# Kernel tuning notes

Hardware: AMD Instinct MI355X
Metric: run time of the kernel (lower is better)

Reference implementation:

```python
import jax, jax.numpy as jnp
import numpy as np

B, T = 256, 2048
D = 64           # rnn_embd_dims (== input_dims)
LB = 2           # len(band_names)
DB = D // LB     # band_embedding_dims = 32
L = 2            # rnn_layers
G = 3 * DB       # GRU gate width


def setup_inputs() -> dict:
    key = jax.random.key(0)
    ks = jax.random.split(key, 10)
    s = 0.1
    return {
        "band_ids": jax.random.randint(ks[0], (B, T), 0, LB),
        "dtime": jax.random.uniform(ks[1], (B, T, 1), dtype=jnp.float32),
        "z_last": jax.random.normal(ks[2], (B, D), dtype=jnp.float32),
        # per-band params stacked on a leading band axis
        "proj_W": jax.random.normal(ks[3], (LB, D + 1, DB)) * s,
        "proj_b": jnp.zeros((LB, DB)),
        "Wih": jax.random.normal(ks[4], (LB, L, G, DB)) * s,
        "Whh": jax.random.normal(ks[5], (LB, L, G, DB)) * s,
        "bih": jnp.zeros((LB, L, G)),
        "bhh": jnp.zeros((LB, L, G)),
        "mW1": jax.random.normal(ks[6], (LB, DB, DB)) * s,
        "mb1": jnp.zeros((LB, DB)),
        "mW2": jax.random.normal(ks[7], (LB, DB, 1)) * s,
        "mb2": jnp.zeros((LB, 1)),
    }


def _gru_layer(x, mask, Wih, Whh, bih, bhh):
    # x: [B,T,DB], mask: [B,T] bool (True = valid step; invalid steps keep h)
    gx = jnp.einsum('btd,gd->btg', x, Wih) + bih  # precompute input gates [B,T,3*DB]

    def step(h, inp):
        gx_t, m_t = inp                 # [B,G], [B]
        gh = h @ Whh.T + bhh            # [B,G]
        r = jax.nn.sigmoid(gx_t[:, :DB] + gh[:, :DB])
        z = jax.nn.sigmoid(gx_t[:, DB:2 * DB] + gh[:, DB:2 * DB])
        n = jnp.tanh(gx_t[:, 2 * DB:] + r * gh[:, 2 * DB:])
        hn = (1.0 - z) * n + z * h
        h = jnp.where(m_t[:, None], hn, h)
        return h, h

    h0 = jnp.zeros((x.shape[0], DB), x.dtype)
    _, ys = jax.lax.scan(step, h0, (gx.transpose(1, 0, 2), mask.T))
    return ys.transpose(1, 0, 2)  # [B,T,DB]


def _forward(band_ids, dtime, z_last, proj_W, proj_b, Wih, Whh, bih, bhh, mW1, mb1, mW2, mb2):
    Bn, Tn = band_ids.shape
    outs = []
    for kb in range(LB):
        mask = band_ids == kb  # [B,T]
        # serial_to_parallel: stable-compact valid steps to the front of each row
        order = jnp.argsort(jnp.logical_not(mask), axis=1, stable=True)
        p_mask = jnp.take_along_axis(mask, order, axis=1)
        p_dtime = jnp.take_along_axis(dtime, order[:, :, None], axis=1)
        # dz = z_last tiled over t; gather along t is identity for a t-constant tensor
        p_dz = jnp.broadcast_to(z_last[:, None, :], (Bn, Tn, z_last.shape[-1]))
        x = jnp.concatenate([p_dz, p_dtime], axis=-1) @ proj_W[kb] + proj_b[kb]
        for l in range(L):
            x = _gru_layer(x, p_mask, Wih[kb, l], Whh[kb, l], bih[kb, l], bhh[kb, l])
        # dz_projection MLP: hidden relu layer + linear head -> [B,T,1]
        y = jax.nn.relu(x @ mW1[kb] + mb1[kb]) @ mW2[kb] + mb2[kb]
        outs.append(y)
    return tuple(outs)


def reference(band_ids, dtime, z_last, proj_W, proj_b, Wih, Whh, bih, bhh, mW1, mb1, mW2, mb2):
    return _forward(band_ids, dtime, z_last, proj_W, proj_b, Wih, Whh, bih, bhh, mW1, mb1, mW2, mb2)
```

## Files before the change

kernel.cpp:

```cpp
#include <hip/hip_runtime.h>


typedef float v2f __attribute__((ext_vector_type(2)));

constexpr int Bn  = 256;
constexpr int Tn  = 2048;
constexpr int Dn  = 64;
constexpr int DBn = 32;
constexpr int Ln  = 2;
constexpr int Gn  = 96;
constexpr int Kc  = 32;

#if __has_builtin(__builtin_amdgcn_exp2f)
__device__ __forceinline__ float exp2_fast(float x) { return __builtin_amdgcn_exp2f(x); }
#else
__device__ __forceinline__ float exp2_fast(float x) { return exp2f(x); }
#endif
#if __has_builtin(__builtin_amdgcn_rcpf)
__device__ __forceinline__ float rcp_fast(float x) { return __builtin_amdgcn_rcpf(x); }
#else
__device__ __forceinline__ float rcp_fast(float x) { return 1.0f / x; }
#endif

__device__ __forceinline__ float sigmoid_f(float x) {
  return rcp_fast(1.0f + exp2_fast(-1.4426950408889634f * x));
}
__device__ __forceinline__ float tanh_f(float x) {
  return 1.0f - 2.0f * rcp_fast(1.0f + exp2_fast(2.8853900817779268f * x));
}

template <int CTRL>
__device__ __forceinline__ float dpp_add(float x) {
  int y = __builtin_amdgcn_update_dpp(0, __builtin_bit_cast(int, x), CTRL, 0xf, 0xf, true);
  return x + __builtin_bit_cast(float, y);
}
__device__ __forceinline__ float dppx8_add(float x) { return dpp_add<0x128>(x); }
__device__ __forceinline__ float dpp_row_sum16(float x) {
  x = dpp_add<0x128>(x);
  x = dpp_add<0x124>(x);
  x = dpp_add<0x122>(x);
  x = dpp_add<0x121>(x);
  return x;
}

__device__ __forceinline__ float dot8(const v2f* __restrict__ w, const v2f* __restrict__ h) {
  v2f a = {0.0f, 0.0f};
  #pragma unroll
  for (int q = 0; q < 8; ++q) a = __builtin_elementwise_fma(w[q], h[q], a);
  return a.x + a.y;
}
__device__ __forceinline__ float dot8b(const v2f* __restrict__ w, const v2f* __restrict__ h) {
  v2f a = {0.0f, 0.0f}, b = {0.0f, 0.0f};
  #pragma unroll
  for (int q = 0; q < 4; ++q) {
    a = __builtin_elementwise_fma(w[q], h[q], a);
    b = __builtin_elementwise_fma(w[q + 4], h[q + 4], b);
  }
  a = a + b;
  return a.x + a.y;
}

__device__ __forceinline__ void ld16(const float* p, v2f* d) {
  #pragma unroll
  for (int q = 0; q < 4; ++q) {
    float4 a = ((const float4*)p)[q];
    d[2*q] = (v2f){a.x, a.y}; d[2*q+1] = (v2f){a.z, a.w};
  }
}

__global__ __launch_bounds__(256, 1)
void rnn_decoder(const int* __restrict__ band_ids, const float* __restrict__ dtime,
                 const float* __restrict__ z_last, const float* __restrict__ projW,
                 const float* __restrict__ projB, const float* __restrict__ Wih,
                 const float* __restrict__ Whh, const float* __restrict__ bih,
                 const float* __restrict__ bhh, const float* __restrict__ mW1,
                 const float* __restrict__ mb1, const float* __restrict__ mW2,
                 const float* __restrict__ mb2, float* __restrict__ out) {
  const int b    = blockIdx.x >> 1;
  const int kb   = blockIdx.x & 1;
  const int tid  = threadIdx.x;
  const int w    = tid >> 6;
  const int L    = tid & 63;
  const int e    = (L & 7) | ((L >> 4) << 3);
  const int koff = ((L >> 3) & 1) * 16;

  __shared__ __align__(16) float yd[Tn];
  __shared__ __align__(16) float gxr_[2][Kc][DBn][4];
  __shared__ __align__(16) float h1r_[2][Kc][DBn];
  __shared__ __align__(16) float h2r_[2][Kc][DBn];
  __shared__ __align__(16) float vr_[2][Kc][4];
  __shared__ __align__(16) float xb[DBn], xs[DBn];
  __shared__ int nsh;

  const float mb2v = mb2[kb];

  if (w == 0) {
    {
      const int*   brow = band_ids + b * Tn;
      const float* drow = dtime    + b * Tn;
      int cnt = 0;
      int4 bcache[8];
      #pragma unroll
      for (int it = 0; it < 8; ++it) {
        int4 v = ((const int4*)(brow + L * 32))[it];
        bcache[it] = v;
        cnt += (v.x == kb) + (v.y == kb) + (v.z == kb) + (v.w == kb);
      }
      int incl = cnt;
      #pragma unroll
      for (int dlt = 1; dlt < 64; dlt <<= 1) {
        int v = __shfl_up(incl, dlt, 64);
        if (L >= dlt) incl += v;
      }
      int off = incl - cnt;
      const int n0 = __shfl(incl, 63, 64);
      #pragma unroll
      for (int it = 0; it < 8; ++it) {
        int4   v  = bcache[it];
        float4 dd = ((const float4*)(drow + L * 32))[it];
        if (v.x == kb) yd[off++] = dd.x;
        if (v.y == kb) yd[off++] = dd.y;
        if (v.z == kb) yd[off++] = dd.z;
        if (v.w == kb) yd[off++] = dd.w;
      }
      if (L == 0) nsh = n0;
    }
    {
      const float* pw = projW + (kb * (Dn + 1)) * DBn + e;
      const float* zl = z_last + b * Dn;
      float acc = 0.0f;
      #pragma unroll 8
      for (int k = 0; k < Dn; ++k) acc = fmaf(zl[k], pw[k * DBn], acc);
      xb[e] = acc + projB[kb * DBn + e];
      xs[e] = pw[Dn * DBn];
    }
    __builtin_amdgcn_wave_barrier();
    const float* wih1  = Wih + ((kb * Ln + 0) * Gn) * DBn;
    const float* bih1p = bih + (kb * Ln + 0) * Gn;
    const float* bhh1p = bhh + (kb * Ln + 0) * Gn;
    float gb_r = 0, gb_z = 0, gb_n = 0, gs_r = 0, gs_z = 0, gs_n = 0;
    #pragma unroll 4
    for (int j = 0; j < DBn; ++j) {
      float xbv = xb[j], xsv = xs[j];
      float wr = wih1[(     e) * DBn + j];
      float wz = wih1[(32 + e) * DBn + j];
      float wn = wih1[(64 + e) * DBn + j];
      gb_r = fmaf(wr, xbv, gb_r);  gs_r = fmaf(wr, xsv, gs_r);
      gb_z = fmaf(wz, xbv, gb_z);  gs_z = fmaf(wz, xsv, gs_z);
      gb_n = fmaf(wn, xbv, gb_n);  gs_n = fmaf(wn, xsv, gs_n);
    }
    gb_r += bih1p[e]      + bhh1p[e];
    gb_z += bih1p[32 + e] + bhh1p[32 + e];
    gb_n += bih1p[64 + e];
    const float bhh1n = bhh1p[64 + e];
    v2f w1r[8], w1z[8], w1n[8];
    const float* whh1 = Whh + ((kb * Ln + 0) * Gn) * DBn;
    ld16(whh1 + (     e) * DBn + koff, w1r);
    ld16(whh1 + (32 + e) * DBn + koff, w1z);
    ld16(whh1 + (64 + e) * DBn + koff, w1n);
    __syncthreads();

#if __has_builtin(__builtin_amdgcn_s_setprio)
    __builtin_amdgcn_s_setprio(1);
#endif
    const int n = nsh;
    const int C = (n + Kc - 1) >> 5;
    v2f h1a[8];
    #pragma unroll
    for (int q = 0; q < 8; ++q) h1a[q] = (v2f){0.0f, 0.0f};
    float h1self = 0.0f;
    for (int c = 0; c < C + 4; ++c) {
      if (c < C) {
        float* ring = &h1r_[c & 1][0][0];
        const int t0 = c * Kc;
        for (int k = 0; k < Kc; ++k) {
          float d  = yd[t0 + k];
          float ar = dot8b(w1r, h1a);
          float az = dot8b(w1z, h1a);
          float an = dot8b(w1n, h1a);
          ar = dppx8_add(ar);
          az = dppx8_add(az);
          an = dppx8_add(an);
          float r1 = sigmoid_f(fmaf(d, gs_r, gb_r) + ar);
          float z1 = sigmoid_f(fmaf(d, gs_z, gb_z) + az);
          float n1 = tanh_f(fmaf(d, gs_n, gb_n) + r1 * (an + bhh1n));
          h1self = fmaf(z1, h1self - n1, n1);
          ring[k * DBn + e] = h1self;
          __builtin_amdgcn_wave_barrier();
          ld16(&ring[k * DBn + koff], h1a);
        }
      }
      __syncthreads();
    }
  } else if (w == 1) {
    const float* wih2 = Wih + ((kb * Ln + 1) * Gn) * DBn;
    v2f wa[8], wbv[8], wcv[8];
    ld16(wih2 + (     e) * DBn + koff, wa);
    ld16(wih2 + (32 + e) * DBn + koff, wbv);
    ld16(wih2 + (64 + e) * DBn + koff, wcv);
    __syncthreads();

    const int n = nsh;
    const int C = (n + Kc - 1) >> 5;
    for (int c = 0; c < C + 4; ++c) {
      if (c >= 1 && c <= C) {
        const int cp = c - 1;
        const float* hsrc = &h1r_[cp & 1][0][0];
        for (int k = 0; k < Kc; ++k) {
          v2f hb[8];
          ld16(&hsrc[k * DBn + koff], hb);
          float g0 = dot8(wa,  hb);
          float g1 = dot8(wbv, hb);
          float g2 = dot8(wcv, hb);
          g0 = dppx8_add(g0);
          g1 = dppx8_add(g1);
          g2 = dppx8_add(g2);
          float4 gv; gv.x = g0; gv.y = g1; gv.z = g2; gv.w = 0.0f;
          *(float4*)&gxr_[cp & 1][k][e][0] = gv;
        }
      }
      if (c >= 4) {
        const int cd = c - 4;
        if (cd < C && L < 32) {
          float4 p = *(const float4*)&vr_[cd & 1][L][0];
          yd[cd * Kc + L] = ((p.x + p.y) + (p.z + p.w)) + mb2v;
        }
      }
      __syncthreads();
    }
  } else if (w == 2) {
    const float* whh2  = Whh + ((kb * Ln + 1) * Gn) * DBn;
    const float* bih2p = bih + (kb * Ln + 1) * Gn;
    const float* bhh2p = bhh + (kb * Ln + 1) * Gn;
    v2f r2w[8], z2w[8], n2w[8];
    ld16(whh2 + (     e) * DBn + koff, r2w);
    ld16(whh2 + (32 + e) * DBn + koff, z2w);
    ld16(whh2 + (64 + e) * DBn + koff, n2w);
    const float c2r   = bih2p[e]      + bhh2p[e];
    const float c2z   = bih2p[32 + e] + bhh2p[32 + e];
    const float bih2n = bih2p[64 + e];
    const float bhh2n = bhh2p[64 + e];
    __syncthreads();

#if __has_builtin(__builtin_amdgcn_s_setprio)
    __builtin_amdgcn_s_setprio(1);
#endif
    const int n = nsh;
    const int C = (n + Kc - 1) >> 5;
    v2f h2a[8];
    #pragma unroll
    for (int q = 0; q < 8; ++q) h2a[q] = (v2f){0.0f, 0.0f};
    float h2self = 0.0f;
    for (int c = 0; c < C + 4; ++c) {
      if (c >= 2 && c <= C + 1) {
        const int cc = c - 2;
        float* ring = &h2r_[cc & 1][0][0];
        for (int k = 0; k < Kc; ++k) {
          float4 g = *(const float4*)&gxr_[cc & 1][k][e][0];
          float cr = dot8b(r2w, h2a);
          float cz = dot8b(z2w, h2a);
          float cn = dot8b(n2w, h2a);
          cr = dppx8_add(cr);
          cz = dppx8_add(cz);
          cn = dppx8_add(cn);
          float r2v = sigmoid_f(g.x + cr + c2r);
          float z2v = sigmoid_f(g.y + cz + c2z);
          float n2v = tanh_f(g.z + bih2n + r2v * (cn + bhh2n));
          h2self = fmaf(z2v, h2self - n2v, n2v);
          ring[k * DBn + e] = h2self;
          __builtin_amdgcn_wave_barrier();
          ld16(&ring[k * DBn + koff], h2a);
        }
      }
      __syncthreads();
    }
  } else {
    v2f m1c[8];
    #pragma unroll
    for (int q = 0; q < 8; ++q)
      m1c[q] = (v2f){ mW1[(kb * DBn + koff + 2*q)     * DBn + e],
                      mW1[(kb * DBn + koff + 2*q + 1) * DBn + e] };
    const float mb1e = mb1[kb * DBn + e];
    const float mW2h = 0.5f * mW2[kb * DBn + e];
    {
      float p = fmaxf(mb1e, 0.0f) * mW2h;
      p = dpp_row_sum16(p);
      if ((L & 15) == 15) vr_[0][L >> 4][(L >> 4) & 3] = p;
    }
    {
      float p = fmaxf(mb1e, 0.0f) * mW2h;
      p = dpp_row_sum16(p);
      if ((L & 15) == 15) vr_[0][0][L >> 4] = p;
    }
    __syncthreads();

    const int n = nsh;
    const int C = (n + Kc - 1) >> 5;
    for (int c = 0; c < C + 4; ++c) {
      if (c >= 3 && c <= C + 2) {
        const int cm = c - 3;
        const float* hsrc = &h2r_[cm & 1][0][0];
        for (int k = 0; k < Kc; ++k) {
          v2f hb[8];
          ld16(&hsrc[k * DBn + koff], hb);
          float mh = dot8(m1c, hb);
          mh = dppx8_add(mh);
          float v = fmaxf(mh + mb1e, 0.0f) * mW2h;
          v = dpp_row_sum16(v);
          if ((L & 15) == 15) vr_[cm & 1][k][L >> 4] = v;
        }
      }
      __syncthreads();
    }
  }

  const int n = nsh;
  float ylast;
  if (n > 0) {
    ylast = yd[n - 1];
  } else {
    float4 p = *(const float4*)&vr_[0][0][0];
    ylast = ((p.x + p.y) + (p.z + p.w)) + mb2v;
  }
  for (int t = n + tid; t < Tn; t += 256) yd[t] = ylast;
  __syncthreads();

  float* orow = out + (kb * Bn + b) * Tn;
  for (int q = tid; q < Tn / 4; q += 256)
    ((float4*)orow)[q] = ((const float4*)yd)[q];
}

extern "C" void kernel_launch(void* const* d_in, const int* in_sizes, int n_in,
                              void* d_out, int out_size, void* d_ws, size_t ws_size,
                              hipStream_t stream) {
  const int*   band_ids = (const int*)  d_in[0];
  const float* dtime    = (const float*)d_in[1];
  const float* z_last   = (const float*)d_in[2];
  const float* projW    = (const float*)d_in[3];
  const float* projB    = (const float*)d_in[4];
  const float* Wih      = (const float*)d_in[5];
  const float* Whh      = (const float*)d_in[6];
  const float* bihp     = (const float*)d_in[7];
  const float* bhhp     = (const float*)d_in[8];
  const float* mW1      = (const float*)d_in[9];
  const float* mb1      = (const float*)d_in[10];
  const float* mW2      = (const float*)d_in[11];
  const float* mb2      = (const float*)d_in[12];
  float* out = (float*)d_out;
  rnn_decoder<<<dim3(Bn * 2), dim3(256), 0, stream>>>(
      band_ids, dtime, z_last, projW, projB, Wih, Whh, bihp, bhhp,
      mW1, mb1, mW2, mb2, out);
}
```

Measured before the change: 325.5 us.

## Merge four-wave pipeline into two waves fusing input-gate and MLP work

Shrinks each block from four waves to two. The layer-1 recurrence wave also computes the layer-2 input-gate projection from its own hidden state, one step behind. The layer-2 recurrence wave also computes the MLP head output in the same way. The shared-memory hidden-state ring buffers become single-step buffers and the pipeline depth drops from four chunks to two, which cuts barrier stages and LDS traffic. The trade-off is more ALU work on the serial critical-path waves, and setprio is removed.

```diff
diff --git a/kernel.cpp b/kernel.cpp
--- a/kernel.cpp
+++ b/kernel.cpp
@@ -68,7 +68,7 @@
   }
 }
 
-__global__ __launch_bounds__(256, 1)
+__global__ __launch_bounds__(128, 1)
 void rnn_decoder(const int* __restrict__ band_ids, const float* __restrict__ dtime,
                  const float* __restrict__ z_last, const float* __restrict__ projW,
                  const float* __restrict__ projB, const float* __restrict__ Wih,
@@ -86,10 +86,11 @@
 
   __shared__ __align__(16) float yd[Tn];
   __shared__ __align__(16) float gxr_[2][Kc][DBn][4];
-  __shared__ __align__(16) float h1r_[2][Kc][DBn];
-  __shared__ __align__(16) float h2r_[2][Kc][DBn];
   __shared__ __align__(16) float vr_[2][Kc][4];
+  __shared__ __align__(16) float h1b[DBn];
+  __shared__ __align__(16) float h2b[DBn];
   __shared__ __align__(16) float xb[DBn], xs[DBn];
+  __shared__ __align__(16) float y0f[4];
   __shared__ int nsh;
 
   const float mb2v = mb2[kb];
@@ -158,21 +159,23 @@
     ld16(whh1 + (     e) * DBn + koff, w1r);
     ld16(whh1 + (32 + e) * DBn + koff, w1z);
     ld16(whh1 + (64 + e) * DBn + koff, w1n);
+    v2f ua[8], ub[8], uc[8];
+    const float* wih2 = Wih + ((kb * Ln + 1) * Gn) * DBn;
+    ld16(wih2 + (     e) * DBn + koff, ua);
+    ld16(wih2 + (32 + e) * DBn + koff, ub);
+    ld16(wih2 + (64 + e) * DBn + koff, uc);
     __syncthreads();
 
-#if __has_builtin(__builtin_amdgcn_s_setprio)
-    __builtin_amdgcn_s_setprio(1);
-#endif
     const int n = nsh;
     const int C = (n + Kc - 1) >> 5;
     v2f h1a[8];
     #pragma unroll
     for (int q = 0; q < 8; ++q) h1a[q] = (v2f){0.0f, 0.0f};
     float h1self = 0.0f;
-    for (int c = 0; c < C + 4; ++c) {
+    for (int c = 0; c < C + 2; ++c) {
       if (c < C) {
-        float* ring = &h1r_[c & 1][0][0];
         const int t0 = c * Kc;
+        float* gxo = &gxr_[c & 1][0][0][0];
         for (int k = 0; k < Kc; ++k) {
           float d  = yd[t0 + k];
           float ar = dot8b(w1r, h1a);
@@ -184,43 +187,35 @@
           float r1 = sigmoid_f(fmaf(d, gs_r, gb_r) + ar);
           float z1 = sigmoid_f(fmaf(d, gs_z, gb_z) + az);
           float n1 = tanh_f(fmaf(d, gs_n, gb_n) + r1 * (an + bhh1n));
-          h1self = fmaf(z1, h1self - n1, n1);
-          ring[k * DBn + e] = h1self;
+          float h1new = fmaf(z1, h1self - n1, n1);
+          h1b[e] = h1new;
           __builtin_amdgcn_wave_barrier();
-          ld16(&ring[k * DBn + koff], h1a);
-        }
-      }
-      __syncthreads();
-    }
-  } else if (w == 1) {
-    const float* wih2 = Wih + ((kb * Ln + 1) * Gn) * DBn;
-    v2f wa[8], wbv[8], wcv[8];
-    ld16(wih2 + (     e) * DBn + koff, wa);
-    ld16(wih2 + (32 + e) * DBn + koff, wbv);
-    ld16(wih2 + (64 + e) * DBn + koff, wcv);
-    __syncthreads();
-
-    const int n = nsh;
-    const int C = (n + Kc - 1) >> 5;
-    for (int c = 0; c < C + 4; ++c) {
-      if (c >= 1 && c <= C) {
-        const int cp = c - 1;
-        const float* hsrc = &h1r_[cp & 1][0][0];
-        for (int k = 0; k < Kc; ++k) {
-          v2f hb[8];
-          ld16(&hsrc[k * DBn + koff], hb);
-          float g0 = dot8(wa,  hb);
-          float g1 = dot8(wbv, hb);
-          float g2 = dot8(wcv, hb);
+          if (k >= 1) {
+            float g0 = dot8(ua, h1a);
+            float g1 = dot8(ub, h1a);
+            float g2 = dot8(uc, h1a);
+            g0 = dppx8_add(g0);
+            g1 = dppx8_add(g1);
+            g2 = dppx8_add(g2);
+            float4 gv; gv.x = g0; gv.y = g1; gv.z = g2; gv.w = 0.0f;
+            *(float4*)&gxo[(k - 1) * DBn * 4 + e * 4] = gv;
+          }
+          h1self = h1new;
+          ld16(&h1b[koff], h1a);
+        }
+        {
+          float g0 = dot8(ua, h1a);
+          float g1 = dot8(ub, h1a);
+          float g2 = dot8(uc, h1a);
           g0 = dppx8_add(g0);
           g1 = dppx8_add(g1);
           g2 = dppx8_add(g2);
           float4 gv; gv.x = g0; gv.y = g1; gv.z = g2; gv.w = 0.0f;
-          *(float4*)&gxr_[cp & 1][k][e][0] = gv;
-        }
-      }
-      if (c >= 4) {
-        const int cd = c - 4;
+          *(float4*)&gxo[(Kc - 1) * DBn * 4 + e * 4] = gv;
+        }
+      }
+      if (c >= 2) {
+        const int cd = c - 2;
         if (cd < C && L < 32) {
           float4 p = *(const float4*)&vr_[cd & 1][L][0];
           yd[cd * Kc + L] = ((p.x + p.y) + (p.z + p.w)) + mb2v;
@@ -228,35 +223,43 @@
       }
       __syncthreads();
     }
-  } else if (w == 2) {
+  } else {
     const float* whh2  = Whh + ((kb * Ln + 1) * Gn) * DBn;
     const float* bih2p = bih + (kb * Ln + 1) * Gn;
     const float* bhh2p = bhh + (kb * Ln + 1) * Gn;
-    v2f r2w[8], z2w[8], n2w[8];
+    v2f r2w[8], z2w[8], n2w[8], m1c[8];
     ld16(whh2 + (     e) * DBn + koff, r2w);
     ld16(whh2 + (32 + e) * DBn + koff, z2w);
     ld16(whh2 + (64 + e) * DBn + koff, n2w);
+    #pragma unroll
+    for (int q = 0; q < 8; ++q)
+      m1c[q] = (v2f){ mW1[(kb * DBn + koff + 2*q)     * DBn + e],
+                      mW1[(kb * DBn + koff + 2*q + 1) * DBn + e] };
     const float c2r   = bih2p[e]      + bhh2p[e];
     const float c2z   = bih2p[32 + e] + bhh2p[32 + e];
     const float bih2n = bih2p[64 + e];
     const float bhh2n = bhh2p[64 + e];
+    const float mb1e  = mb1[kb * DBn + e];
+    const float mW2h  = 0.5f * mW2[kb * DBn + e];
+    {
+      float p = fmaxf(mb1e, 0.0f) * mW2h;
+      p = dpp_row_sum16(p);
+      if ((L & 15) == 15) y0f[L >> 4] = p;
+    }
     __syncthreads();
 
-#if __has_builtin(__builtin_amdgcn_s_setprio)
-    __builtin_amdgcn_s_setprio(1);
-#endif
     const int n = nsh;
     const int C = (n + Kc - 1) >> 5;
     v2f h2a[8];
     #pragma unroll
     for (int q = 0; q < 8; ++q) h2a[q] = (v2f){0.0f, 0.0f};
     float h2self = 0.0f;
-    for (int c = 0; c < C + 4; ++c) {
-      if (c >= 2 && c <= C + 1) {
-        const int cc = c - 2;
-        float* ring = &h2r_[cc & 1][0][0];
+    for (int c = 0; c < C + 2; ++c) {
+      if (c >= 1 && c <= C) {
+        const int cc = c - 1;
+        const float* gx = &gxr_[cc & 1][0][0][0];
         for (int k = 0; k < Kc; ++k) {
-          float4 g = *(const float4*)&gxr_[cc & 1][k][e][0];
+          float4 g = *(const float4*)&gx[k * DBn * 4 + e * 4];
           float cr = dot8b(r2w, h2a);
           float cz = dot8b(z2w, h2a);
           float cn = dot8b(n2w, h2a);
@@ -266,48 +269,25 @@
           float r2v = sigmoid_f(g.x + cr + c2r);
           float z2v = sigmoid_f(g.y + cz + c2z);
           float n2v = tanh_f(g.z + bih2n + r2v * (cn + bhh2n));
-          h2self = fmaf(z2v, h2self - n2v, n2v);
-          ring[k * DBn + e] = h2self;
+          float h2new = fmaf(z2v, h2self - n2v, n2v);
+          h2b[e] = h2new;
           __builtin_amdgcn_wave_barrier();
-          ld16(&ring[k * DBn + koff], h2a);
-        }
-      }
-      __syncthreads();
-    }
-  } else {
-    v2f m1c[8];
-    #pragma unroll
-    for (int q = 0; q < 8; ++q)
-      m1c[q] = (v2f){ mW1[(kb * DBn + koff + 2*q)     * DBn + e],
-                      mW1[(kb * DBn + koff + 2*q + 1) * DBn + e] };
-    const float mb1e = mb1[kb * DBn + e];
-    const float mW2h = 0.5f * mW2[kb * DBn + e];
-    {
-      float p = fmaxf(mb1e, 0.0f) * mW2h;
-      p = dpp_row_sum16(p);
-      if ((L & 15) == 15) vr_[0][L >> 4][(L >> 4) & 3] = p;
-    }
-    {
-      float p = fmaxf(mb1e, 0.0f) * mW2h;
-      p = dpp_row_sum16(p);
-      if ((L & 15) == 15) vr_[0][0][L >> 4] = p;
-    }
-    __syncthreads();
-
-    const int n = nsh;
-    const int C = (n + Kc - 1) >> 5;
-    for (int c = 0; c < C + 4; ++c) {
-      if (c >= 3 && c <= C + 2) {
-        const int cm = c - 3;
-        const float* hsrc = &h2r_[cm & 1][0][0];
-        for (int k = 0; k < Kc; ++k) {
-          v2f hb[8];
-          ld16(&hsrc[k * DBn + koff], hb);
-          float mh = dot8(m1c, hb);
+          if (k >= 1) {
+            float mh = dot8(m1c, h2a);
+            mh = dppx8_add(mh);
+            float v = fmaxf(mh + mb1e, 0.0f) * mW2h;
+            v = dpp_row_sum16(v);
+            if ((L & 15) == 15) vr_[cc & 1][k - 1][L >> 4] = v;
+          }
+          h2self = h2new;
+          ld16(&h2b[koff], h2a);
+        }
+        {
+          float mh = dot8(m1c, h2a);
           mh = dppx8_add(mh);
           float v = fmaxf(mh + mb1e, 0.0f) * mW2h;
           v = dpp_row_sum16(v);
-          if ((L & 15) == 15) vr_[cm & 1][k][L >> 4] = v;
+          if ((L & 15) == 15) vr_[cc & 1][Kc - 1][L >> 4] = v;
         }
       }
       __syncthreads();
@@ -319,14 +299,14 @@
   if (n > 0) {
     ylast = yd[n - 1];
   } else {
-    float4 p = *(const float4*)&vr_[0][0][0];
+    float4 p = *(const float4*)&y0f[0];
     ylast = ((p.x + p.y) + (p.z + p.w)) + mb2v;
   }
-  for (int t = n + tid; t < Tn; t += 256) yd[t] = ylast;
+  for (int t = n + tid; t < Tn; t += 128) yd[t] = ylast;
   __syncthreads();
 
   float* orow = out + (kb * Bn + b) * Tn;
-  for (int q = tid; q < Tn / 4; q += 256)
+  for (int q = tid; q < Tn / 4; q += 128)
     ((float4*)orow)[q] = ((const float4*)yd)[q];
 }
 
@@ -347,7 +327,7 @@
   const float* mW2      = (const float*)d_in[11];
   const float* mb2      = (const float*)d_in[12];
   float* out = (float*)d_out;
-  rnn_decoder<<<dim3(Bn * 2), dim3(256), 0, stream>>>(
+  rnn_decoder<<<dim3(Bn * 2), dim3(128), 0, stream>>>(
       band_ids, dtime, z_last, projW, projB, Wih, Whh, bihp, bhhp,
       mW1, mb1, mW2, mb2, out);
 }
```

After: 478.3 us. 46.9% more time.

## Fuse MLP head into layer-2 GRU wave and shorten pipeline to three waves

Applied to the files above, without the earlier changes.

The wave that ran the dz-projection MLP is removed. Its MLP is now computed inside the layer-2 GRU wave, one step behind, using a ping-pong of register copies of h2 in place of the h2 shared-memory ring. The block shrinks to 192 threads and the chunk pipeline loses one stage, which reduces pipeline fill/drain and barrier work. The layer-1 loop also reads dtime four steps at a time. The exchange is that the serial layer-2 recurrence now carries extra MLP arithmetic on its critical path.

```diff
diff --git a/kernel.cpp b/kernel.cpp
--- a/kernel.cpp
+++ b/kernel.cpp
@@ -68,7 +68,7 @@
   }
 }
 
-__global__ __launch_bounds__(256, 1)
+__global__ __launch_bounds__(192, 1)
 void rnn_decoder(const int* __restrict__ band_ids, const float* __restrict__ dtime,
                  const float* __restrict__ z_last, const float* __restrict__ projW,
                  const float* __restrict__ projB, const float* __restrict__ Wih,
@@ -87,9 +87,10 @@
   __shared__ __align__(16) float yd[Tn];
   __shared__ __align__(16) float gxr_[2][Kc][DBn][4];
   __shared__ __align__(16) float h1r_[2][Kc][DBn];
-  __shared__ __align__(16) float h2r_[2][Kc][DBn];
   __shared__ __align__(16) float vr_[2][Kc][4];
+  __shared__ __align__(16) float h2b[DBn];
   __shared__ __align__(16) float xb[DBn], xs[DBn];
+  __shared__ __align__(16) float y0f[4];
   __shared__ int nsh;
 
   const float mb2v = mb2[kb];
@@ -169,25 +170,29 @@
     #pragma unroll
     for (int q = 0; q < 8; ++q) h1a[q] = (v2f){0.0f, 0.0f};
     float h1self = 0.0f;
-    for (int c = 0; c < C + 4; ++c) {
+    for (int c = 0; c < C + 3; ++c) {
       if (c < C) {
         float* ring = &h1r_[c & 1][0][0];
         const int t0 = c * Kc;
-        for (int k = 0; k < Kc; ++k) {
-          float d  = yd[t0 + k];
-          float ar = dot8b(w1r, h1a);
-          float az = dot8b(w1z, h1a);
-          float an = dot8b(w1n, h1a);
-          ar = dppx8_add(ar);
-          az = dppx8_add(az);
-          an = dppx8_add(an);
-          float r1 = sigmoid_f(fmaf(d, gs_r, gb_r) + ar);
-          float z1 = sigmoid_f(fmaf(d, gs_z, gb_z) + az);
-          float n1 = tanh_f(fmaf(d, gs_n, gb_n) + r1 * (an + bhh1n));
-          h1self = fmaf(z1, h1self - n1, n1);
-          ring[k * DBn + e] = h1self;
-          __builtin_amdgcn_wave_barrier();
-          ld16(&ring[k * DBn + koff], h1a);
+        for (int k = 0; k < Kc; k += 4) {
+          float4 d4 = *(const float4*)&yd[t0 + k];
+          #pragma unroll
+          for (int u = 0; u < 4; ++u) {
+            float d  = (u == 0) ? d4.x : (u == 1) ? d4.y : (u == 2) ? d4.z : d4.w;
+            float ar = dot8b(w1r, h1a);
+            float az = dot8b(w1z, h1a);
+            float an = dot8b(w1n, h1a);
+            ar = dppx8_add(ar);
+            az = dppx8_add(az);
+            an = dppx8_add(an);
+            float r1 = sigmoid_f(fmaf(d, gs_r, gb_r) + ar);
+            float z1 = sigmoid_f(fmaf(d, gs_z, gb_z) + az);
+            float n1 = tanh_f(fmaf(d, gs_n, gb_n) + r1 * (an + bhh1n));
+            h1self = fmaf(z1, h1self - n1, n1);
+            ring[(k + u) * DBn + e] = h1self;
+            __builtin_amdgcn_wave_barrier();
+            ld16(&ring[(k + u) * DBn + koff], h1a);
+          }
         }
       }
       __syncthreads();
@@ -202,7 +207,7 @@
 
     const int n = nsh;
     const int C = (n + Kc - 1) >> 5;
-    for (int c = 0; c < C + 4; ++c) {
+    for (int c = 0; c < C + 3; ++c) {
       if (c >= 1 && c <= C) {
         const int cp = c - 1;
         const float* hsrc = &h1r_[cp & 1][0][0];
@@ -219,8 +224,8 @@
           *(float4*)&gxr_[cp & 1][k][e][0] = gv;
         }
       }
-      if (c >= 4) {
-        const int cd = c - 4;
+      if (c >= 3) {
+        const int cd = c - 3;
         if (cd < C && L < 32) {
           float4 p = *(const float4*)&vr_[cd & 1][L][0];
           yd[cd * Kc + L] = ((p.x + p.y) + (p.z + p.w)) + mb2v;
@@ -228,18 +233,29 @@
       }
       __syncthreads();
     }
-  } else if (w == 2) {
+  } else {
     const float* whh2  = Whh + ((kb * Ln + 1) * Gn) * DBn;
     const float* bih2p = bih + (kb * Ln + 1) * Gn;
     const float* bhh2p = bhh + (kb * Ln + 1) * Gn;
-    v2f r2w[8], z2w[8], n2w[8];
+    v2f r2w[8], z2w[8], n2w[8], m1c[8];
     ld16(whh2 + (     e) * DBn + koff, r2w);
     ld16(whh2 + (32 + e) * DBn + koff, z2w);
     ld16(whh2 + (64 + e) * DBn + koff, n2w);
+    #pragma unroll
+    for (int q = 0; q < 8; ++q)
+      m1c[q] = (v2f){ mW1[(kb * DBn + koff + 2*q)     * DBn + e],
+                      mW1[(kb * DBn + koff + 2*q + 1) * DBn + e] };
     const float c2r   = bih2p[e]      + bhh2p[e];
     const float c2z   = bih2p[32 + e] + bhh2p[32 + e];
     const float bih2n = bih2p[64 + e];
     const float bhh2n = bhh2p[64 + e];
+    const float mb1e  = mb1[kb * DBn + e];
+    const float mW2h  = 0.5f * mW2[kb * DBn + e];
+    {
+      float p = fmaxf(mb1e, 0.0f) * mW2h;
+      p = dpp_row_sum16(p);
+      if ((L & 15) == 15) y0f[L >> 4] = p;
+    }
     __syncthreads();
 
 #if __has_builtin(__builtin_amdgcn_s_setprio)
@@ -247,71 +263,55 @@
 #endif
     const int n = nsh;
     const int C = (n + Kc - 1) >> 5;
-    v2f h2a[8];
+    v2f h2A[8], h2B[8];
     #pragma unroll
-    for (int q = 0; q < 8; ++q) h2a[q] = (v2f){0.0f, 0.0f};
+    for (int q = 0; q < 8; ++q) { h2A[q] = (v2f){0.0f, 0.0f}; h2B[q] = (v2f){0.0f, 0.0f}; }
     float h2self = 0.0f;
-    for (int c = 0; c < C + 4; ++c) {
+
+#define L2_STEP(K, CUR, NXT)                                                   \
+    {                                                                          \
+      float4 g = *(const float4*)&gxr_[cc & 1][(K)][e][0];                     \
+      float cr = dot8b(r2w, CUR);                                              \
+      float cz = dot8b(z2w, CUR);                                              \
+      float cn = dot8b(n2w, CUR);                                              \
+      cr = dppx8_add(cr);                                                      \
+      cz = dppx8_add(cz);                                                      \
+      cn = dppx8_add(cn);                                                      \
+      float r2v = sigmoid_f(g.x + cr + c2r);                                   \
+      float z2v = sigmoid_f(g.y + cz + c2z);                                   \
+      float n2v = tanh_f(g.z + bih2n + r2v * (cn + bhh2n));                    \
+      float h2new = fmaf(z2v, h2self - n2v, n2v);                              \
+      h2b[e] = h2new;                                                          \
+      __builtin_amdgcn_wave_barrier();                                         \
+      ld16(&h2b[koff], NXT);                                                   \
+      if ((K) >= 1) {                                                          \
+        float mh = dot8(m1c, CUR);                                             \
+        mh = dppx8_add(mh);                                                    \
+        float v = fmaxf(mh + mb1e, 0.0f) * mW2h;                               \
+        v = dpp_row_sum16(v);                                                  \
+        if ((L & 15) == 15) vr_[cc & 1][(K) - 1][L >> 4] = v;                  \
+      }                                                                        \
+      h2self = h2new;                                                          \
+    }
+
+    for (int c = 0; c < C + 3; ++c) {
       if (c >= 2 && c <= C + 1) {
         const int cc = c - 2;
-        float* ring = &h2r_[cc & 1][0][0];
-        for (int k = 0; k < Kc; ++k) {
-          float4 g = *(const float4*)&gxr_[cc & 1][k][e][0];
-          float cr = dot8b(r2w, h2a);
-          float cz = dot8b(z2w, h2a);
-          float cn = dot8b(n2w, h2a);
-          cr = dppx8_add(cr);
-          cz = dppx8_add(cz);
-          cn = dppx8_add(cn);
-          float r2v = sigmoid_f(g.x + cr + c2r);
-          float z2v = sigmoid_f(g.y + cz + c2z);
-          float n2v = tanh_f(g.z + bih2n + r2v * (cn + bhh2n));
-          h2self = fmaf(z2v, h2self - n2v, n2v);
-          ring[k * DBn + e] = h2self;
-          __builtin_amdgcn_wave_barrier();
-          ld16(&ring[k * DBn + koff], h2a);
-        }
-      }
-      __syncthreads();
-    }
-  } else {
-    v2f m1c[8];
-    #pragma unroll
-    for (int q = 0; q < 8; ++q)
-      m1c[q] = (v2f){ mW1[(kb * DBn + koff + 2*q)     * DBn + e],
-                      mW1[(kb * DBn + koff + 2*q + 1) * DBn + e] };
-    const float mb1e = mb1[kb * DBn + e];
-    const float mW2h = 0.5f * mW2[kb * DBn + e];
-    {
-      float p = fmaxf(mb1e, 0.0f) * mW2h;
-      p = dpp_row_sum16(p);
-      if ((L & 15) == 15) vr_[0][L >> 4][(L >> 4) & 3] = p;
-    }
-    {
-      float p = fmaxf(mb1e, 0.0f) * mW2h;
-      p = dpp_row_sum16(p);
-      if ((L & 15) == 15) vr_[0][0][L >> 4] = p;
-    }
-    __syncthreads();
-
-    const int n = nsh;
-    const int C = (n + Kc - 1) >> 5;
-    for (int c = 0; c < C + 4; ++c) {
-      if (c >= 3 && c <= C + 2) {
-        const int cm = c - 3;
-        const float* hsrc = &h2r_[cm & 1][0][0];
-        for (int k = 0; k < Kc; ++k) {
-          v2f hb[8];
-          ld16(&hsrc[k * DBn + koff], hb);
-          float mh = dot8(m1c, hb);
+        for (int k = 0; k < Kc; k += 2) {
+          L2_STEP(k,     h2A, h2B)
+          L2_STEP(k + 1, h2B, h2A)
+        }
+        {
+          float mh = dot8(m1c, h2A);
           mh = dppx8_add(mh);
           float v = fmaxf(mh + mb1e, 0.0f) * mW2h;
           v = dpp_row_sum16(v);
-          if ((L & 15) == 15) vr_[cm & 1][k][L >> 4] = v;
+          if ((L & 15) == 15) vr_[cc & 1][Kc - 1][L >> 4] = v;
         }
       }
       __syncthreads();
     }
+#undef L2_STEP
   }
 
   const int n = nsh;
@@ -319,14 +319,14 @@
   if (n > 0) {
     ylast = yd[n - 1];
   } else {
-    float4 p = *(const float4*)&vr_[0][0][0];
+    float4 p = *(const float4*)&y0f[0];
     ylast = ((p.x + p.y) + (p.z + p.w)) + mb2v;
   }
-  for (int t = n + tid; t < Tn; t += 256) yd[t] = ylast;
+  for (int t = n + tid; t < Tn; t += 192) yd[t] = ylast;
   __syncthreads();
 
   float* orow = out + (kb * Bn + b) * Tn;
-  for (int q = tid; q < Tn / 4; q += 256)
+  for (int q = tid; q < Tn / 4; q += 192)
     ((float4*)orow)[q] = ((const float4*)yd)[q];
 }
 
@@ -347,7 +347,7 @@
   const float* mW2      = (const float*)d_in[11];
   const float* mb2      = (const float*)d_in[12];
   float* out = (float*)d_out;
-  rnn_decoder<<<dim3(Bn * 2), dim3(256), 0, stream>>>(
+  rnn_decoder<<<dim3(Bn * 2), dim3(192), 0, stream>>>(
       band_ids, dtime, z_last, projW, projB, Wih, Whh, bihp, bhhp,
       mW1, mb1, mW2, mb2, out);
 }
```

Measured after the change: 425.4 us. +30.7%, slower.

## Remap lanes so each lane owns two outputs with 4-way K split

Applied to the files above, without the earlier changes.

Changes the per-wave lane mapping from 2-way K split with one output element per lane to a 4-way K split with two output elements per lane (e and e+16). Each lane now does half-length dot products per gate and reduces across 4 lanes with two DPP adds. The recurrent h reload per step shrinks to 8 floats, and the layer-1 loop reads dtime as float4 and unrolls by 4. The aim is to shorten the serial per-step dependency chain in the GRU recurrences, at the cost of twice as many gate activations per lane and more registers.

```diff
diff --git a/kernel.cpp b/kernel.cpp
--- a/kernel.cpp
+++ b/kernel.cpp
@@ -34,38 +34,27 @@
   int y = __builtin_amdgcn_update_dpp(0, __builtin_bit_cast(int, x), CTRL, 0xf, 0xf, true);
   return x + __builtin_bit_cast(float, y);
 }
-__device__ __forceinline__ float dppx8_add(float x) { return dpp_add<0x128>(x); }
-__device__ __forceinline__ float dpp_row_sum16(float x) {
+__device__ __forceinline__ float comb48(float x) {
+  x = dpp_add<0x124>(x);
   x = dpp_add<0x128>(x);
-  x = dpp_add<0x124>(x);
-  x = dpp_add<0x122>(x);
-  x = dpp_add<0x121>(x);
   return x;
 }
 
-__device__ __forceinline__ float dot8(const v2f* __restrict__ w, const v2f* __restrict__ h) {
-  v2f a = {0.0f, 0.0f};
-  #pragma unroll
-  for (int q = 0; q < 8; ++q) a = __builtin_elementwise_fma(w[q], h[q], a);
-  return a.x + a.y;
-}
-__device__ __forceinline__ float dot8b(const v2f* __restrict__ w, const v2f* __restrict__ h) {
+__device__ __forceinline__ float dot4(const v2f* __restrict__ w, const v2f* __restrict__ h) {
   v2f a = {0.0f, 0.0f}, b = {0.0f, 0.0f};
-  #pragma unroll
-  for (int q = 0; q < 4; ++q) {
-    a = __builtin_elementwise_fma(w[q], h[q], a);
-    b = __builtin_elementwise_fma(w[q + 4], h[q + 4], b);
-  }
+  a = __builtin_elementwise_fma(w[0], h[0], a);
+  b = __builtin_elementwise_fma(w[1], h[1], b);
+  a = __builtin_elementwise_fma(w[2], h[2], a);
+  b = __builtin_elementwise_fma(w[3], h[3], b);
   a = a + b;
   return a.x + a.y;
 }
 
-__device__ __forceinline__ void ld16(const float* p, v2f* d) {
-  #pragma unroll
-  for (int q = 0; q < 4; ++q) {
-    float4 a = ((const float4*)p)[q];
-    d[2*q] = (v2f){a.x, a.y}; d[2*q+1] = (v2f){a.z, a.w};
-  }
+__device__ __forceinline__ void ld8(const float* p, v2f* d) {
+  float4 a = ((const float4*)p)[0];
+  float4 bq = ((const float4*)p)[1];
+  d[0] = (v2f){a.x, a.y};  d[1] = (v2f){a.z, a.w};
+  d[2] = (v2f){bq.x, bq.y}; d[3] = (v2f){bq.z, bq.w};
 }
 
 __global__ __launch_bounds__(256, 1)
@@ -81,8 +70,10 @@
   const int tid  = threadIdx.x;
   const int w    = tid >> 6;
   const int L    = tid & 63;
-  const int e    = (L & 7) | ((L >> 4) << 3);
-  const int koff = ((L >> 3) & 1) * 16;
+  const int row  = L >> 4;
+  const int kq   = (L >> 2) & 3;
+  const int e    = (L & 3) | (row << 2);
+  const int ko   = kq * 8;
 
   __shared__ __align__(16) float yd[Tn];
   __shared__ __align__(16) float gxr_[2][Kc][DBn][4];
@@ -90,6 +81,7 @@
   __shared__ __align__(16) float h2r_[2][Kc][DBn];
   __shared__ __align__(16) float vr_[2][Kc][4];
   __shared__ __align__(16) float xb[DBn], xs[DBn];
+  __shared__ __align__(16) float y0f[4];
   __shared__ int nsh;
 
   const float mb2v = mb2[kb];
@@ -126,38 +118,56 @@
       if (L == 0) nsh = n0;
     }
     {
-      const float* pw = projW + (kb * (Dn + 1)) * DBn + e;
       const float* zl = z_last + b * Dn;
-      float acc = 0.0f;
-      #pragma unroll 8
-      for (int k = 0; k < Dn; ++k) acc = fmaf(zl[k], pw[k * DBn], acc);
-      xb[e] = acc + projB[kb * DBn + e];
-      xs[e] = pw[Dn * DBn];
+      #pragma unroll
+      for (int s = 0; s < 2; ++s) {
+        const int ee = e + 16 * s;
+        const float* pw = projW + (kb * (Dn + 1)) * DBn + ee;
+        float acc = 0.0f;
+        #pragma unroll 8
+        for (int k = 0; k < Dn; ++k) acc = fmaf(zl[k], pw[k * DBn], acc);
+        xb[ee] = acc + projB[kb * DBn + ee];
+        xs[ee] = pw[Dn * DBn];
+      }
     }
     __builtin_amdgcn_wave_barrier();
     const float* wih1  = Wih + ((kb * Ln + 0) * Gn) * DBn;
     const float* bih1p = bih + (kb * Ln + 0) * Gn;
     const float* bhh1p = bhh + (kb * Ln + 0) * Gn;
-    float gb_r = 0, gb_z = 0, gb_n = 0, gs_r = 0, gs_z = 0, gs_n = 0;
+    float gb_r0 = 0, gb_z0 = 0, gb_n0 = 0, gs_r0 = 0, gs_z0 = 0, gs_n0 = 0;
+    float gb_r1 = 0, gb_z1 = 0, gb_n1 = 0, gs_r1 = 0, gs_z1 = 0, gs_n1 = 0;
     #pragma unroll 4
     for (int j = 0; j < DBn; ++j) {
       float xbv = xb[j], xsv = xs[j];
-      float wr = wih1[(     e) * DBn + j];
-      float wz = wih1[(32 + e) * DBn + j];
-      float wn = wih1[(64 + e) * DBn + j];
-      gb_r = fmaf(wr, xbv, gb_r);  gs_r = fmaf(wr, xsv, gs_r);
-      gb_z = fmaf(wz, xbv, gb_z);  gs_z = fmaf(wz, xsv, gs_z);
-      gb_n = fmaf(wn, xbv, gb_n);  gs_n = fmaf(wn, xsv, gs_n);
-    }
-    gb_r += bih1p[e]      + bhh1p[e];
-    gb_z += bih1p[32 + e] + bhh1p[32 + e];
-    gb_n += bih1p[64 + e];
-    const float bhh1n = bhh1p[64 + e];
-    v2f w1r[8], w1z[8], w1n[8];
+      float a0 = wih1[(      e) * DBn + j];
+      float a1 = wih1[(32 +  e) * DBn + j];
+      float a2 = wih1[(64 +  e) * DBn + j];
+      float b0 = wih1[(16 +  e) * DBn + j];
+      float b1 = wih1[(48 +  e) * DBn + j];
+      float b2 = wih1[(80 +  e) * DBn + j];
+      gb_r0 = fmaf(a0, xbv, gb_r0);  gs_r0 = fmaf(a0, xsv, gs_r0);
+      gb_z0 = fmaf(a1, xbv, gb_z0);  gs_z0 = fmaf(a1, xsv, gs_z0);
+      gb_n0 = fmaf(a2, xbv, gb_n0);  gs_n0 = fmaf(a2, xsv, gs_n0);
+      gb_r1 = fmaf(b0, xbv, gb_r1);  gs_r1 = fmaf(b0, xsv, gs_r1);
+      gb_z1 = fmaf(b1, xbv, gb_z1);  gs_z1 = fmaf(b1, xsv, gs_z1);
+      gb_n1 = fmaf(b2, xbv, gb_n1);  gs_n1 = fmaf(b2, xsv, gs_n1);
+    }
+    gb_r0 += bih1p[e]      + bhh1p[e];
+    gb_z0 += bih1p[32 + e] + bhh1p[32 + e];
+    gb_n0 += bih1p[64 + e];
+    gb_r1 += bih1p[16 + e] + bhh1p[16 + e];
+    gb_z1 += bih1p[48 + e] + bhh1p[48 + e];
+    gb_n1 += bih1p[80 + e];
+    const float bhh1n0 = bhh1p[64 + e];
+    const float bhh1n1 = bhh1p[80 + e];
+    v2f w1r0[4], w1z0[4], w1n0[4], w1r1[4], w1z1[4], w1n1[4];
     const float* whh1 = Whh + ((kb * Ln + 0) * Gn) * DBn;
-    ld16(whh1 + (     e) * DBn + koff, w1r);
-    ld16(whh1 + (32 + e) * DBn + koff, w1z);
-    ld16(whh1 + (64 + e) * DBn + koff, w1n);
+    ld8(whh1 + (      e) * DBn + ko, w1r0);
+    ld8(whh1 + (32 +  e) * DBn + ko, w1z0);
+    ld8(whh1 + (64 +  e) * DBn + ko, w1n0);
+    ld8(whh1 + (16 +  e) * DBn + ko, w1r1);
+    ld8(whh1 + (48 +  e) * DBn + ko, w1z1);
+    ld8(whh1 + (80 +  e) * DBn + ko, w1n1);
     __syncthreads();
 
 #if __has_builtin(__builtin_amdgcn_s_setprio)
@@ -165,39 +175,51 @@
 #endif
     const int n = nsh;
     const int C = (n + Kc - 1) >> 5;
-    v2f h1a[8];
+    v2f h1a[4];
     #pragma unroll
-    for (int q = 0; q < 8; ++q) h1a[q] = (v2f){0.0f, 0.0f};
-    float h1self = 0.0f;
+    for (int q = 0; q < 4; ++q) h1a[q] = (v2f){0.0f, 0.0f};
+    float h1s0 = 0.0f, h1s1 = 0.0f;
     for (int c = 0; c < C + 4; ++c) {
       if (c < C) {
         float* ring = &h1r_[c & 1][0][0];
         const int t0 = c * Kc;
-        for (int k = 0; k < Kc; ++k) {
-          float d  = yd[t0 + k];
-          float ar = dot8b(w1r, h1a);
-          float az = dot8b(w1z, h1a);
-          float an = dot8b(w1n, h1a);
-          ar = dppx8_add(ar);
-          az = dppx8_add(az);
-          an = dppx8_add(an);
-          float r1 = sigmoid_f(fmaf(d, gs_r, gb_r) + ar);
-          float z1 = sigmoid_f(fmaf(d, gs_z, gb_z) + az);
-          float n1 = tanh_f(fmaf(d, gs_n, gb_n) + r1 * (an + bhh1n));
-          h1self = fmaf(z1, h1self - n1, n1);
-          ring[k * DBn + e] = h1self;
-          __builtin_amdgcn_wave_barrier();
-          ld16(&ring[k * DBn + koff], h1a);
+        for (int k = 0; k < Kc; k += 4) {
+          float4 d4 = *(const float4*)&yd[t0 + k];
+          #pragma unroll
+          for (int u = 0; u < 4; ++u) {
+            float d  = (u == 0) ? d4.x : (u == 1) ? d4.y : (u == 2) ? d4.z : d4.w;
+            float ar0 = comb48(dot4(w1r0, h1a));
+            float az0 = comb48(dot4(w1z0, h1a));
+            float an0 = comb48(dot4(w1n0, h1a));
+            float ar1 = comb48(dot4(w1r1, h1a));
+            float az1 = comb48(dot4(w1z1, h1a));
+            float an1 = comb48(dot4(w1n1, h1a));
+            float r10 = sigmoid_f(fmaf(d, gs_r0, gb_r0) + ar0);
+            float z10 = sigmoid_f(fmaf(d, gs_z0, gb_z0) + az0);
+            float n10 = tanh_f(fmaf(d, gs_n0, gb_n0) + r10 * (an0 + bhh1n0));
+            float r11v = sigmoid_f(fmaf(d, gs_r1, gb_r1) + ar1);
+            float z11v = sigmoid_f(fmaf(d, gs_z1, gb_z1) + az1);
+            float n11v = tanh_f(fmaf(d, gs_n1, gb_n1) + r11v * (an1 + bhh1n1));
+            h1s0 = fmaf(z10,  h1s0 - n10,  n10);
+            h1s1 = fmaf(z11v, h1s1 - n11v, n11v);
+            ring[(k + u) * DBn + e]      = h1s0;
+            ring[(k + u) * DBn + e + 16] = h1s1;
+            __builtin_amdgcn_wave_barrier();
+            ld8(&ring[(k + u) * DBn + ko], h1a);
+          }
         }
       }
       __syncthreads();
     }
   } else if (w == 1) {
     const float* wih2 = Wih + ((kb * Ln + 1) * Gn) * DBn;
-    v2f wa[8], wbv[8], wcv[8];
-    ld16(wih2 + (     e) * DBn + koff, wa);
-    ld16(wih2 + (32 + e) * DBn + koff, wbv);
-    ld16(wih2 + (64 + e) * DBn + koff, wcv);
+    v2f ua0[4], uz0[4], un0[4], ua1[4], uz1[4], un1[4];
+    ld8(wih2 + (      e) * DBn + ko, ua0);
+    ld8(wih2 + (32 +  e) * DBn + ko, uz0);
+    ld8(wih2 + (64 +  e) * DBn + ko, un0);
+    ld8(wih2 + (16 +  e) * DBn + ko, ua1);
+    ld8(wih2 + (48 +  e) * DBn + ko, uz1);
+    ld8(wih2 + (80 +  e) * DBn + ko, un1);
     __syncthreads();
 
     const int n = nsh;
@@ -207,16 +229,18 @@
         const int cp = c - 1;
         const float* hsrc = &h1r_[cp & 1][0][0];
         for (int k = 0; k < Kc; ++k) {
-          v2f hb[8];
-          ld16(&hsrc[k * DBn + koff], hb);
-          float g0 = dot8(wa,  hb);
-          float g1 = dot8(wbv, hb);
-          float g2 = dot8(wcv, hb);
-          g0 = dppx8_add(g0);
-          g1 = dppx8_add(g1);
-          g2 = dppx8_add(g2);
-          float4 gv; gv.x = g0; gv.y = g1; gv.z = g2; gv.w = 0.0f;
-          *(float4*)&gxr_[cp & 1][k][e][0] = gv;
+          v2f hb[4];
+          ld8(&hsrc[k * DBn + ko], hb);
+          float g0 = comb48(dot4(ua0, hb));
+          float g1 = comb48(dot4(uz0, hb));
+          float g2 = comb48(dot4(un0, hb));
+          float g3 = comb48(dot4(ua1, hb));
+          float g4 = comb48(dot4(uz1, hb));
+          float g5 = comb48(dot4(un1, hb));
+          float4 gv0; gv0.x = g0; gv0.y = g1; gv0.z = g2; gv0.w = 0.0f;
+          float4 gv1; gv1.x = g3; gv1.y = g4; gv1.z = g5; gv1.w = 0.0f;
+          *(float4*)&gxr_[cp & 1][k][e][0]      = gv0;
+          *(float4*)&gxr_[cp & 1][k][e + 16][0] = gv1;
         }
       }
       if (c >= 4) {
@@ -232,14 +256,21 @@
     const float* whh2  = Whh + ((kb * Ln + 1) * Gn) * DBn;
     const float* bih2p = bih + (kb * Ln + 1) * Gn;
     const float* bhh2p = bhh + (kb * Ln + 1) * Gn;
-    v2f r2w[8], z2w[8], n2w[8];
-    ld16(whh2 + (     e) * DBn + koff, r2w);
-    ld16(whh2 + (32 + e) * DBn + koff, z2w);
-    ld16(whh2 + (64 + e) * DBn + koff, n2w);
-    const float c2r   = bih2p[e]      + bhh2p[e];
-    const float c2z   = bih2p[32 + e] + bhh2p[32 + e];
-    const float bih2n = bih2p[64 + e];
-    const float bhh2n = bhh2p[64 + e];
+    v2f r2w0[4], z2w0[4], n2w0[4], r2w1[4], z2w1[4], n2w1[4];
+    ld8(whh2 + (      e) * DBn + ko, r2w0);
+    ld8(whh2 + (32 +  e) * DBn + ko, z2w0);
+    ld8(whh2 + (64 +  e) * DBn + ko, n2w0);
+    ld8(whh2 + (16 +  e) * DBn + ko, r2w1);
+    ld8(whh2 + (48 +  e) * DBn + ko, z2w1);
+    ld8(whh2 + (80 +  e) * DBn + ko, n2w1);
+    const float c2r0   = bih2p[e]      + bhh2p[e];
+    const float c2z0   = bih2p[32 + e] + bhh2p[32 + e];
+    const float bih2n0 = bih2p[64 + e];
+    const float bhh2n0 = bhh2p[64 + e];
+    const float c2r1   = bih2p[16 + e] + bhh2p[16 + e];
+    const float c2z1   = bih2p[48 + e] + bhh2p[48 + e];
+    const float bih2n1 = bih2p[80 + e];
+    const float bhh2n1 = bhh2p[80 + e];
     __syncthreads();
 
 #if __has_builtin(__builtin_amdgcn_s_setprio)
@@ -247,50 +278,57 @@
 #endif
     const int n = nsh;
     const int C = (n + Kc - 1) >> 5;
-    v2f h2a[8];
+    v2f h2a[4];
     #pragma unroll
-    for (int q = 0; q < 8; ++q) h2a[q] = (v2f){0.0f, 0.0f};
-    float h2self = 0.0f;
+    for (int q = 0; q < 4; ++q) h2a[q] = (v2f){0.0f, 0.0f};
+    float h2s0 = 0.0f, h2s1 = 0.0f;
     for (int c = 0; c < C + 4; ++c) {
       if (c >= 2 && c <= C + 1) {
         const int cc = c - 2;
         float* ring = &h2r_[cc & 1][0][0];
         for (int k = 0; k < Kc; ++k) {
-          float4 g = *(const float4*)&gxr_[cc & 1][k][e][0];
-          float cr = dot8b(r2w, h2a);
-          float cz = dot8b(z2w, h2a);
-          float cn = dot8b(n2w, h2a);
-          cr = dppx8_add(cr);
-          cz = dppx8_add(cz);
-          cn = dppx8_add(cn);
-          float r2v = sigmoid_f(g.x + cr + c2r);
-          float z2v = sigmoid_f(g.y + cz + c2z);
-          float n2v = tanh_f(g.z + bih2n + r2v * (cn + bhh2n));
-          h2self = fmaf(z2v, h2self - n2v, n2v);
-          ring[k * DBn + e] = h2self;
+          float4 g0 = *(const float4*)&gxr_[cc & 1][k][e][0];
+          float4 g1 = *(const float4*)&gxr_[cc & 1][k][e + 16][0];
+          float cr0 = comb48(dot4(r2w0, h2a));
+          float cz0 = comb48(dot4(z2w0, h2a));
+          float cn0 = comb48(dot4(n2w0, h2a));
+          float cr1 = comb48(dot4(r2w1, h2a));
+          float cz1 = comb48(dot4(z2w1, h2a));
+          float cn1 = comb48(dot4(n2w1, h2a));
+          float r20 = sigmoid_f(g0.x + cr0 + c2r0);
+          float z20 = sigmoid_f(g0.y + cz0 + c2z0);
+          float n20 = tanh_f(g0.z + bih2n0 + r20 * (cn0 + bhh2n0));
+          float r21 = sigmoid_f(g1.x + cr1 + c2r1);
+          float z21 = sigmoid_f(g1.y + cz1 + c2z1);
+          float n21 = tanh_f(g1.z + bih2n1 + r21 * (cn1 + bhh2n1));
+          h2s0 = fmaf(z20, h2s0 - n20, n20);
+          h2s1 = fmaf(z21, h2s1 - n21, n21);
+          ring[k * DBn + e]      = h2s0;
+          ring[k * DBn + e + 16] = h2s1;
           __builtin_amdgcn_wave_barrier();
-          ld16(&ring[k * DBn + koff], h2a);
+          ld8(&ring[k * DBn + ko], h2a);
         }
       }
       __syncthreads();
     }
   } else {
-    v2f m1c[8];
+    v2f m1c0[4], m1c1[4];
     #pragma unroll
-    for (int q = 0; q < 8; ++q)
-      m1c[q] = (v2f){ mW1[(kb * DBn + koff + 2*q)     * DBn + e],
-                      mW1[(kb * DBn + koff + 2*q + 1) * DBn + e] };
-    const float mb1e = mb1[kb * DBn + e];
-    const float mW2h = 0.5f * mW2[kb * DBn + e];
+    for (int q = 0; q < 4; ++q) {
+      m1c0[q] = (v2f){ mW1[(kb * DBn + ko + 2*q)     * DBn + e],
+                       mW1[(kb * DBn + ko + 2*q + 1) * DBn + e] };
+      m1c1[q] = (v2f){ mW1[(kb * DBn + ko + 2*q)     * DBn + e + 16],
+                       mW1[(kb * DBn + ko + 2*q + 1) * DBn + e + 16] };
+    }
+    const float mb1e0 = mb1[kb * DBn + e];
+    const float mb1e1 = mb1[kb * DBn + e + 16];
+    const float mW2e0 = mW2[kb * DBn + e];
+    const float mW2e1 = mW2[kb * DBn + e + 16];
     {
-      float p = fmaxf(mb1e, 0.0f) * mW2h;
-      p = dpp_row_sum16(p);
-      if ((L & 15) == 15) vr_[0][L >> 4][(L >> 4) & 3] = p;
-    }
-    {
-      float p = fmaxf(mb1e, 0.0f) * mW2h;
-      p = dpp_row_sum16(p);
-      if ((L & 15) == 15) vr_[0][0][L >> 4] = p;
+      float v = fmaxf(mb1e0, 0.0f) * mW2e0 + fmaxf(mb1e1, 0.0f) * mW2e1;
+      v = dpp_add<0x121>(v);
+      v = dpp_add<0x122>(v);
+      if ((L & 15) == 15) y0f[row] = v;
     }
     __syncthreads();
 
@@ -299,15 +337,18 @@
     for (int c = 0; c < C + 4; ++c) {
       if (c >= 3 && c <= C + 2) {
         const int cm = c - 3;
-        const float* hsrc = &h2r_[cm & 1][0][0];
-        for (int k = 0; k < Kc; ++k) {
-          v2f hb[8];
-          ld16(&hsrc[k * DBn + koff], hb);
-          float mh = dot8(m1c, hb);
-          mh = dppx8_add(mh);
-          float v = fmaxf(mh + mb1e, 0.0f) * mW2h;
-          v = dpp_row_sum16(v);
-          if ((L & 15) == 15) vr_[cm & 1][k][L >> 4] = v;
+        if (cm < C) {
+          const float* hsrc = &h2r_[cm & 1][0][0];
+          for (int k = 0; k < Kc; ++k) {
+            v2f hb[4];
+            ld8(&hsrc[k * DBn + ko], hb);
+            float p0 = comb48(dot4(m1c0, hb));
+            float p1 = comb48(dot4(m1c1, hb));
+            float v = fmaxf(p0 + mb1e0, 0.0f) * mW2e0 + fmaxf(p1 + mb1e1, 0.0f) * mW2e1;
+            v = dpp_add<0x121>(v);
+            v = dpp_add<0x122>(v);
+            if ((L & 15) == 15) vr_[cm & 1][k][row] = v;
+          }
         }
       }
       __syncthreads();
@@ -319,7 +360,7 @@
   if (n > 0) {
     ylast = yd[n - 1];
   } else {
-    float4 p = *(const float4*)&vr_[0][0][0];
+    float4 p = *(const float4*)&y0f[0];
     ylast = ((p.x + p.y) + (p.z + p.w)) + mb2v;
   }
   for (int t = n + tid; t < Tn; t += 256) yd[t] = ylast;
```

After: 463.4 us. +42.4%, slower.
